# Optimization experiments

Hardware: AMD Instinct MI355X
Metric: run time of the kernel (lower is better)

The kernel has to match this reference:

```python
import jax, jax.numpy as jnp
import numpy as np

IN_DIM = 18 * 2 * 1 * 536  # 19296
H = 512
OUT = 11
STEPS = 1024


def setup_inputs() -> dict:
    key = jax.random.key(0)
    ks = jax.random.split(key, 14)
    s = 0.02  # small init scale for stable LSTM dynamics
    f32 = jnp.float32
    return {
        "inputs": jax.random.normal(ks[0], (STEPS, IN_DIM), dtype=f32),
        "W_in": jax.random.normal(ks[1], (H, IN_DIM), dtype=f32) * s,
        "b_in": jnp.zeros((H,), dtype=f32),
        "Wih0": jax.random.normal(ks[2], (4 * H, H), dtype=f32) * s,
        "Whh0": jax.random.normal(ks[3], (4 * H, H), dtype=f32) * s,
        "bih0": jnp.zeros((4 * H,), dtype=f32),
        "bhh0": jnp.zeros((4 * H,), dtype=f32),
        "Wih1": jax.random.normal(ks[4], (4 * H, H), dtype=f32) * s,
        "Whh1": jax.random.normal(ks[5], (4 * H, H), dtype=f32) * s,
        "bih1": jnp.zeros((4 * H,), dtype=f32),
        "bhh1": jnp.zeros((4 * H,), dtype=f32),
        "W_out": jax.random.normal(ks[6], (OUT, H), dtype=f32) * s,
        "b_out": jnp.zeros((OUT,), dtype=f32),
    }


def _lstm_cell(gates, c):
    # PyTorch gate order: input, forget, cell(g), output
    i, f, g, o = jnp.split(gates, 4, axis=-1)
    c_new = jax.nn.sigmoid(f) * c + jax.nn.sigmoid(i) * jnp.tanh(g)
    h_new = jax.nn.sigmoid(o) * jnp.tanh(c_new)
    return h_new, c_new


def reference(inputs, W_in, b_in, Wih0, Whh0, bih0, bhh0,
              Wih1, Whh1, bih1, bhh1, W_out, b_out):
    # Input projection is time-independent -> batch it across all steps.
    x_proj = inputs @ W_in.T + b_in            # (STEPS, H)
    gx0 = x_proj @ Wih0.T + bih0               # (STEPS, 4H) precomputed layer-0 input gates

    def step(carry, gx0_t):
        h0, c0, h1, c1 = carry
        h0, c0 = _lstm_cell(gx0_t + h0 @ Whh0.T + bhh0, c0)
        h1, c1 = _lstm_cell(h0 @ Wih1.T + bih1 + h1 @ Whh1.T + bhh1, c1)
        return (h0, c0, h1, c1), h1

    z = jnp.zeros((H,), dtype=inputs.dtype)
    (h0, c0, h1, c1), hs = jax.lax.scan(step, (z, z, z, z), gx0)
    outputs = (hs @ W_out.T + b_out)[:, None, :]   # (STEPS, 1, OUT) == torch (steps, batch=1, 11)
    hn = jnp.stack([h0, h1])[:, None, :]           # (num_layers=2, batch=1, H)
    cn = jnp.stack([c0, c1])[:, None, :]
    return outputs, hn, cn
```

## Files before the change

kernel.cpp:

```cpp
#include <hip/hip_runtime.h>
#include <math.h>

typedef unsigned long long ull;
typedef unsigned int u32;
typedef unsigned short u16;
typedef _Float16 half2v __attribute__((ext_vector_type(2)));
typedef __bf16 bf16x8 __attribute__((ext_vector_type(8)));
typedef float f32x4 __attribute__((ext_vector_type(4)));

#define H 512
#define STEPS 1024
#define OUTN 11

__device__ __forceinline__ float sigm(float x) { return 1.f / (1.f + __expf(-x)); }
__device__ __forceinline__ ull ld_pair(const ull* p) {
  return __hip_atomic_load((ull*)p, __ATOMIC_RELAXED, __HIP_MEMORY_SCOPE_AGENT);
}
__device__ __forceinline__ void st_pair(ull* p, ull v) {
  __hip_atomic_store(p, v, __ATOMIC_RELAXED, __HIP_MEMORY_SCOPE_AGENT);
}
__device__ __forceinline__ float dot2acc(half2v a, half2v b, float c) {
#if __has_builtin(__builtin_amdgcn_fdot2)
  return __builtin_amdgcn_fdot2(a, b, c, false);
#else
  return c + (float)a.x * (float)b.x + (float)a.y * (float)b.y;
#endif
}
__device__ __forceinline__ u16 f16bits(float x) {
  return __builtin_bit_cast(u16, (_Float16)x);
}
__device__ __forceinline__ half2v bch2(u32 u) { return __builtin_bit_cast(half2v, u); }

__device__ __forceinline__ u32 split_bf16(float x) {
  u32 u = __float_as_uint(x);
  u32 rh = (u + 0x7FFFu + ((u >> 16) & 1u)) & 0xFFFF0000u;
  float hf = __uint_as_float(rh);
  float lo = x - hf;
  u32 ul = __float_as_uint(lo);
  u32 rl = (ul + 0x7FFFu + ((ul >> 16) & 1u)) & 0xFFFF0000u;
  return (rh >> 16) | rl;
}

__global__ void cvt_split(float* __restrict__ A, float* __restrict__ B, int nA, int n4) {
  int idx = blockIdx.x * 256 + threadIdx.x;
  if (idx >= n4) return;
  int base = idx * 4;
  float* p = (base < nA) ? (A + base) : (B + (base - nA));
  float4 v = *(float4*)p;
  u32 r0 = split_bf16(v.x), r1 = split_bf16(v.y), r2 = split_bf16(v.z), r3 = split_bf16(v.w);
  uint4 o = make_uint4(r0, r1, r2, r3);
  *(uint4*)p = o;
}

__global__ __launch_bounds__(256, 2)
void gemm_hilo(const u32* __restrict__ A2, const u32* __restrict__ B2,
               float* __restrict__ C, int M, int N, int K)
{
  __shared__ __align__(16) u16 Ah[64 * 32], Al[64 * 32], Bh[64 * 32], Bl[64 * 32];
  const int z = blockIdx.z;
  const int zstart = z * 151;
  const int nsteps = (z < 3) ? 151 : 150;
  const int mt = blockIdx.x * 64, nt = blockIdx.y * 64;
  const int tid = threadIdx.x;
  const int row = tid >> 2, cg = (tid & 3) * 8;
  const int wave = tid >> 6, lane = tid & 63;
  const int wm = (wave & 1) * 32, wn = (wave >> 1) * 32;
  const int quad = lane >> 4, l16 = lane & 15;

  f32x4 acc[2][2];
#pragma unroll
  for (int i = 0; i < 2; ++i)
#pragma unroll
    for (int j = 0; j < 2; ++j) acc[i][j] = (f32x4)0.f;

  for (int s = 0; s < nsteps; ++s) {
    const int kb = (zstart + s) * 32;
    {
      const u32* ap = A2 + (size_t)(mt + row) * K + kb + cg;
      const u32* bp = B2 + (size_t)(nt + row) * K + kb + cg;
      uint4 a0 = *(const uint4*)ap, a1 = *(const uint4*)(ap + 4);
      uint4 b0 = *(const uint4*)bp, b1 = *(const uint4*)(bp + 4);
      uint4 hi, lo;
      hi = make_uint4((a0.x & 0xFFFF) | (a0.y << 16), (a0.z & 0xFFFF) | (a0.w << 16),
                      (a1.x & 0xFFFF) | (a1.y << 16), (a1.z & 0xFFFF) | (a1.w << 16));
      lo = make_uint4((a0.x >> 16) | (a0.y & 0xFFFF0000u), (a0.z >> 16) | (a0.w & 0xFFFF0000u),
                      (a1.x >> 16) | (a1.y & 0xFFFF0000u), (a1.z >> 16) | (a1.w & 0xFFFF0000u));
      *(uint4*)&Ah[row * 32 + cg] = hi;
      *(uint4*)&Al[row * 32 + cg] = lo;
      hi = make_uint4((b0.x & 0xFFFF) | (b0.y << 16), (b0.z & 0xFFFF) | (b0.w << 16),
                      (b1.x & 0xFFFF) | (b1.y << 16), (b1.z & 0xFFFF) | (b1.w << 16));
      lo = make_uint4((b0.x >> 16) | (b0.y & 0xFFFF0000u), (b0.z >> 16) | (b0.w & 0xFFFF0000u),
                      (b1.x >> 16) | (b1.y & 0xFFFF0000u), (b1.z >> 16) | (b1.w & 0xFFFF0000u));
      *(uint4*)&Bh[row * 32 + cg] = hi;
      *(uint4*)&Bl[row * 32 + cg] = lo;
    }
    __syncthreads();
    bf16x8 ah[2], al[2], bh[2], bl[2];
#pragma unroll
    for (int mf = 0; mf < 2; ++mf) {
      int r = (wm + mf * 16 + l16) * 32 + quad * 8;
      ah[mf] = *reinterpret_cast<const bf16x8*>(&Ah[r]);
      al[mf] = *reinterpret_cast<const bf16x8*>(&Al[r]);
    }
#pragma unroll
    for (int nf = 0; nf < 2; ++nf) {
      int r = (wn + nf * 16 + l16) * 32 + quad * 8;
      bh[nf] = *reinterpret_cast<const bf16x8*>(&Bh[r]);
      bl[nf] = *reinterpret_cast<const bf16x8*>(&Bl[r]);
    }
#pragma unroll
    for (int mf = 0; mf < 2; ++mf)
#pragma unroll
      for (int nf = 0; nf < 2; ++nf) {
        acc[mf][nf] = __builtin_amdgcn_mfma_f32_16x16x32_bf16(ah[mf], bh[nf], acc[mf][nf], 0, 0, 0);
        acc[mf][nf] = __builtin_amdgcn_mfma_f32_16x16x32_bf16(ah[mf], bl[nf], acc[mf][nf], 0, 0, 0);
        acc[mf][nf] = __builtin_amdgcn_mfma_f32_16x16x32_bf16(al[mf], bh[nf], acc[mf][nf], 0, 0, 0);
      }
    __syncthreads();
  }

#pragma unroll
  for (int mf = 0; mf < 2; ++mf)
#pragma unroll
    for (int nf = 0; nf < 2; ++nf)
#pragma unroll
      for (int r = 0; r < 4; ++r) {
        int rw = mt + wm + mf * 16 + quad * 4 + r;
        int cl = nt + wn + nf * 16 + l16;
        atomicAdd(&C[(size_t)rw * N + cl], acc[mf][nf][r]);
      }
}

#define GBM 64
#define GBN 64
#define GBK 64
#define GLD 76

__global__ __launch_bounds__(256, 2)
void gemm_nt(const float* __restrict__ A, const float* __restrict__ B,
             float* __restrict__ C, const float* __restrict__ bias,
             int M, int N, int K)
{
  __shared__ float As[GBM][GLD];
  __shared__ float Bs[GBN][GLD];
  const int mt = blockIdx.x, nt = blockIdx.y;
  const int tid = threadIdx.x;
  const int tx = tid & 15, ty = tid >> 4;

  float acc[4][4] = {{0.f}};

  for (int kb = 0; kb < K; kb += GBK) {
#pragma unroll
    for (int i = 0; i < 4; ++i) {
      int r = ty + i * 16;
      int gk = kb + tx * 4;
      *(float4*)&As[r][tx * 4] = *(const float4*)(A + (size_t)(mt * GBM + r) * K + gk);
      *(float4*)&Bs[r][tx * 4] = *(const float4*)(B + (size_t)(nt * GBN + r) * K + gk);
    }
    __syncthreads();
#pragma unroll
    for (int k4 = 0; k4 < GBK; k4 += 4) {
      float4 a[4], b[4];
#pragma unroll
      for (int i = 0; i < 4; ++i) a[i] = *(const float4*)&As[ty * 4 + i][k4];
#pragma unroll
      for (int j = 0; j < 4; ++j) b[j] = *(const float4*)&Bs[tx * 4 + j][k4];
#pragma unroll
      for (int i = 0; i < 4; ++i)
#pragma unroll
        for (int j = 0; j < 4; ++j) {
          acc[i][j] = fmaf(a[i].x, b[j].x, acc[i][j]);
          acc[i][j] = fmaf(a[i].y, b[j].y, acc[i][j]);
          acc[i][j] = fmaf(a[i].z, b[j].z, acc[i][j]);
          acc[i][j] = fmaf(a[i].w, b[j].w, acc[i][j]);
        }
    }
    __syncthreads();
  }

#pragma unroll
  for (int i = 0; i < 4; ++i) {
    int m = mt * GBM + ty * 4 + i;
#pragma unroll
    for (int j = 0; j < 4; ++j) {
      int n = nt * GBN + tx * 4 + j;
      C[(size_t)m * N + n] = acc[i][j] + bias[n];
    }
  }
}

__global__ void init_xproj(float* __restrict__ xp, const float* __restrict__ b_in) {
  int i = blockIdx.x * 256 + threadIdx.x;
  xp[i] = b_in[i & (H - 1)];
}

__global__ void out_proj(const float* __restrict__ hs1, const float* __restrict__ Wout,
                         const float* __restrict__ bout, float* __restrict__ out) {
  int idx = blockIdx.x * 256 + threadIdx.x;
  if (idx >= STEPS * OUTN) return;
  int t = idx / OUTN, o = idx - t * OUTN;
  const float* h = hs1 + t * H;
  const float* wr = Wout + o * H;
  float acc = 0.f;
#pragma unroll 4
  for (int i = 0; i < H; i += 4) {
    float4 hv = *(const float4*)(h + i);
    float4 wv = *(const float4*)(wr + i);
    acc = fmaf(hv.x, wv.x, acc);
    acc = fmaf(hv.y, wv.y, acc);
    acc = fmaf(hv.z, wv.z, acc);
    acc = fmaf(hv.w, wv.w, acc);
  }
  out[idx] = acc + bout[o];
}

__global__ __launch_bounds__(512, 1)
void lstm_chains(const float* __restrict__ gx0,
                 const float* __restrict__ Whh0, const float* __restrict__ bhh0,
                 const float* __restrict__ Wih1, const float* __restrict__ Whh1,
                 const float* __restrict__ bih1, const float* __restrict__ bhh1,
                 float* __restrict__ hs1, float* __restrict__ out,
                 ull* __restrict__ hb0, ull* __restrict__ hb1,
                 int* __restrict__ flags1)
{
  const int wg = blockIdx.x;
  const int tid = threadIdx.x;
  const bool role0 = (wg < 8);

  __shared__ __align__(16) u32 hl_u[512];
  __shared__ __align__(16) float gbuf[256];
  __shared__ __align__(16) float gxb[256];

  half2v wgt[8][16];
  float bias[8];
  int rg, ch;

  if (role0) {
    rg = tid >> 4; ch = tid & 15;
    int g = rg >> 3, lub = (rg & 7) * 8;
    int growb = (g << 9) + (wg << 6) + lub;
    const float* wb = Whh0 + (size_t)growb * H + ch * 32;
#pragma unroll
    for (int r = 0; r < 8; ++r) {
      const float* wr = wb + (size_t)r * H;
#pragma unroll
      for (int j4 = 0; j4 < 8; ++j4) {
        float4 f = *(const float4*)(wr + j4 * 4);
        wgt[r][2 * j4]     = half2v{(_Float16)f.x, (_Float16)f.y};
        wgt[r][2 * j4 + 1] = half2v{(_Float16)f.z, (_Float16)f.w};
      }
      bias[r] = bhh0[growb + r];
    }
  } else {
    rg = tid >> 5; ch = tid & 31;
    int g = rg >> 2, lub = (rg & 3) * 8;
    int growb = (g << 9) + ((wg - 8) << 5) + lub;
    const float* wb = (ch < 16) ? (Whh1 + (size_t)growb * H + ch * 32)
                                : (Wih1 + (size_t)growb * H + (ch - 16) * 32);
#pragma unroll
    for (int r = 0; r < 8; ++r) {
      const float* wr = wb + (size_t)r * H;
#pragma unroll
      for (int j4 = 0; j4 < 8; ++j4) {
        float4 f = *(const float4*)(wr + j4 * 4);
        wgt[r][2 * j4]     = half2v{(_Float16)f.x, (_Float16)f.y};
        wgt[r][2 * j4 + 1] = half2v{(_Float16)f.z, (_Float16)f.w};
      }
      bias[r] = bih1[growb + r] + bhh1[growb + r];
    }
  }

  float c_state = 0.f, h_last = 0.f;

  if (role0) {
    const int w = wg;
    for (int t = 0; t < STEPS; ++t) {
      if (tid >= 256) {
        int j = tid - 256;
        gxb[j] = gx0[t * 2048 + ((j >> 6) << 9) + (w << 6) + (j & 63)];
      } else {
        const ull* src = hb0 + (((unsigned)(t + 3) & 3u) << 8) + tid;
        ull p;
        do { p = ld_pair(src); } while ((unsigned)(p >> 32) != (unsigned)t);
        hl_u[tid] = (u32)p;
      }
      __syncthreads();

      float accv[8];
#pragma unroll
      for (int r = 0; r < 8; ++r) accv[r] = 0.f;
      {
        const u32* hp = hl_u + (ch << 4);
        uint4 q0 = *(const uint4*)hp;
        uint4 q1 = *(const uint4*)(hp + 4);
        uint4 q2 = *(const uint4*)(hp + 8);
        uint4 q3 = *(const uint4*)(hp + 12);
        half2v h2[16] = {bch2(q0.x), bch2(q0.y), bch2(q0.z), bch2(q0.w),
                         bch2(q1.x), bch2(q1.y), bch2(q1.z), bch2(q1.w),
                         bch2(q2.x), bch2(q2.y), bch2(q2.z), bch2(q2.w),
                         bch2(q3.x), bch2(q3.y), bch2(q3.z), bch2(q3.w)};
#pragma unroll
        for (int j = 0; j < 16; ++j)
#pragma unroll
          for (int r = 0; r < 8; ++r)
            accv[r] = dot2acc(wgt[r][j], h2[j], accv[r]);
      }
#pragma unroll
      for (int o = 1; o < 16; o <<= 1)
#pragma unroll
        for (int r = 0; r < 8; ++r)
          accv[r] += __shfl_xor(accv[r], o);
      if (ch == 0) {
        float4 ga = *(const float4*)&gxb[rg * 8];
        float4 gb = *(const float4*)&gxb[rg * 8 + 4];
        float4 o0 = make_float4(accv[0] + bias[0] + ga.x, accv[1] + bias[1] + ga.y,
                                accv[2] + bias[2] + ga.z, accv[3] + bias[3] + ga.w);
        float4 o1 = make_float4(accv[4] + bias[4] + gb.x, accv[5] + bias[5] + gb.y,
                                accv[6] + bias[6] + gb.z, accv[7] + bias[7] + gb.w);
        *(float4*)&gbuf[rg * 8] = o0;
        *(float4*)&gbuf[rg * 8 + 4] = o1;
      }
      __syncthreads();

      if (tid < 64) {
        float gi = gbuf[tid], gf = gbuf[64 + tid], gg = gbuf[128 + tid], go = gbuf[192 + tid];
        c_state = sigm(gf) * c_state + sigm(gi) * tanhf(gg);
        float hv = sigm(go) * tanhf(c_state);
        h_last = hv;
        int need = t - 3;
        if (need > 0) {
          int f;
          do {
            f = (tid < 16) ? __hip_atomic_load(&flags1[tid], __ATOMIC_RELAXED,
                                               __HIP_MEMORY_SCOPE_AGENT)
                           : 0x7fffffff;
          } while (!__all(f >= need));
        }
        float hnb = __shfl_down(hv, 1);
        if ((tid & 1) == 0) {
          u32 pay = (u32)f16bits(hv) | ((u32)f16bits(hnb) << 16);
          st_pair(hb0 + (((unsigned)t & 3u) << 8) + (w << 5) + (tid >> 1),
                  ((ull)(unsigned)(t + 1) << 32) | (ull)pay);
        }
      }
    }
  } else {
    const int w1 = wg - 8;
    for (int tau = 1; tau <= STEPS; ++tau) {
      const int t = tau - 1;
      if (tid < 256) {
        const ull* q1 = hb1 + (((unsigned)(t + 3) & 3u) << 8) + tid;
        ull p;
        do { p = ld_pair(q1); } while ((unsigned)(p >> 32) != (unsigned)t);
        hl_u[tid] = (u32)p;
      } else {
        const ull* q0 = hb0 + (((unsigned)t & 3u) << 8) + (tid - 256);
        ull p;
        do { p = ld_pair(q0); } while ((unsigned)(p >> 32) != (unsigned)(t + 1));
        hl_u[tid] = (u32)p;
      }
      __syncthreads();

      float accv[8];
#pragma unroll
      for (int r = 0; r < 8; ++r) accv[r] = 0.f;
      {
        const u32* hp = hl_u + (ch << 4);
        uint4 q0 = *(const uint4*)hp;
        uint4 q1 = *(const uint4*)(hp + 4);
        uint4 q2 = *(const uint4*)(hp + 8);
        uint4 q3 = *(const uint4*)(hp + 12);
        half2v h2[16] = {bch2(q0.x), bch2(q0.y), bch2(q0.z), bch2(q0.w),
                         bch2(q1.x), bch2(q1.y), bch2(q1.z), bch2(q1.w),
                         bch2(q2.x), bch2(q2.y), bch2(q2.z), bch2(q2.w),
                         bch2(q3.x), bch2(q3.y), bch2(q3.z), bch2(q3.w)};
#pragma unroll
        for (int j = 0; j < 16; ++j)
#pragma unroll
          for (int r = 0; r < 8; ++r)
            accv[r] = dot2acc(wgt[r][j], h2[j], accv[r]);
      }
#pragma unroll
      for (int o = 1; o < 32; o <<= 1)
#pragma unroll
        for (int r = 0; r < 8; ++r)
          accv[r] += __shfl_xor(accv[r], o);
      if (ch == 0) {
        float4 o0 = make_float4(accv[0] + bias[0], accv[1] + bias[1],
                                accv[2] + bias[2], accv[3] + bias[3]);
        float4 o1 = make_float4(accv[4] + bias[4], accv[5] + bias[5],
                                accv[6] + bias[6], accv[7] + bias[7]);
        *(float4*)&gbuf[rg * 8] = o0;
        *(float4*)&gbuf[rg * 8 + 4] = o1;
      }
      __syncthreads();

      if (tid < 32) {
        int u = (w1 << 5) + tid;
        float gi = gbuf[tid], gf = gbuf[32 + tid], gg = gbuf[64 + tid], go = gbuf[96 + tid];
        c_state = sigm(gf) * c_state + sigm(gi) * tanhf(gg);
        float hv = sigm(go) * tanhf(c_state);
        h_last = hv;
        hs1[t * H + u] = hv;
        float hnb = __shfl_down(hv, 1);
        if ((tid & 1) == 0) {
          u32 pay = (u32)f16bits(hv) | ((u32)f16bits(hnb) << 16);
          st_pair(hb1 + (((unsigned)t & 3u) << 8) + (w1 << 4) + (tid >> 1),
                  ((ull)(unsigned)(t + 1) << 32) | (ull)pay);
        }
      }
      if (tid == 0)
        __hip_atomic_store(&flags1[w1], tau, __ATOMIC_RELAXED, __HIP_MEMORY_SCOPE_AGENT);
    }
  }

  if (role0) {
    if (tid < 64) {
      int u = (wg << 6) + tid;
      out[STEPS * OUTN + u] = h_last;
      out[STEPS * OUTN + 2 * H + u] = c_state;
    }
  } else {
    if (tid < 32) {
      int u = ((wg - 8) << 5) + tid;
      out[STEPS * OUTN + H + u] = h_last;
      out[STEPS * OUTN + 3 * H + u] = c_state;
    }
  }
}

extern "C" void kernel_launch(void* const* d_in, const int* in_sizes, int n_in,
                              void* d_out, int out_size, void* d_ws, size_t ws_size,
                              hipStream_t stream)
{
  (void)in_sizes; (void)n_in; (void)out_size; (void)ws_size;
  float* inputs = (float*)d_in[0];
  float* W_in   = (float*)d_in[1];
  const float* b_in   = (const float*)d_in[2];
  const float* Wih0   = (const float*)d_in[3];
  const float* Whh0   = (const float*)d_in[4];
  const float* bih0   = (const float*)d_in[5];
  const float* bhh0   = (const float*)d_in[6];
  const float* Wih1   = (const float*)d_in[7];
  const float* Whh1   = (const float*)d_in[8];
  const float* bih1   = (const float*)d_in[9];
  const float* bhh1   = (const float*)d_in[10];
  const float* W_out  = (const float*)d_in[11];
  const float* b_out  = (const float*)d_in[12];
  float* out = (float*)d_out;
  float* ws = (float*)d_ws;

  float* xp  = ws;
  float* gx0 = ws + 524288;
  float* hs1 = ws + 524288 + 2097152;
  char* syncb = (char*)(ws + 3145728);
  ull* hb0 = (ull*)syncb;
  ull* hb1 = (ull*)(syncb + 8192);
  int* flags1 = (int*)(syncb + 16384);

  hipMemsetAsync(syncb, 0, 16448, stream);

  {
    const int nA = STEPS * 19296;
    const int n4 = (nA + H * 19296) / 4;
    cvt_split<<<n4 / 256, 256, 0, stream>>>(inputs, W_in, nA, n4);
  }
  init_xproj<<<2048, 256, 0, stream>>>(xp, b_in);
  {
    dim3 g(16, 8, 4);
    gemm_hilo<<<g, 256, 0, stream>>>((const u32*)inputs, (const u32*)W_in, xp,
                                     1024, 512, 19296);
  }
  {
    dim3 g(16, 32, 1);
    gemm_nt<<<g, 256, 0, stream>>>(xp, Wih0, gx0, bih0, 1024, 2048, 512);
  }
  lstm_chains<<<24, 512, 0, stream>>>(gx0, Whh0, bhh0, Wih1, Whh1, bih1, bhh1,
                                      hs1, out, hb0, hb1, flags1);
  out_proj<<<44, 256, 0, stream>>>(hs1, W_out, b_out, out);
}
```

Before: 3.582 ms.

## Replicate hidden-state mailboxes per consumer and deepen ring to eight slots

```diff
diff --git a/kernel.cpp b/kernel.cpp
--- a/kernel.cpp
+++ b/kernel.cpp
@@ -214,13 +214,17 @@
   out[idx] = acc + bout[o];
 }
 
+#define NC0 24
+#define NC1 16
+#define RD 8
+
 __global__ __launch_bounds__(512, 1)
 void lstm_chains(const float* __restrict__ gx0,
                  const float* __restrict__ Whh0, const float* __restrict__ bhh0,
                  const float* __restrict__ Wih1, const float* __restrict__ Whh1,
                  const float* __restrict__ bih1, const float* __restrict__ bhh1,
                  float* __restrict__ hs1, float* __restrict__ out,
-                 ull* __restrict__ hb0, ull* __restrict__ hb1,
+                 ull* __restrict__ mb0, ull* __restrict__ mb1,
                  int* __restrict__ flags1)
 {
   const int wg = blockIdx.x;
@@ -278,8 +282,14 @@
       if (tid >= 256) {
         int j = tid - 256;
         gxb[j] = gx0[t * 2048 + ((j >> 6) << 9) + (w << 6) + (j & 63)];
+        if (j < 16 && (t & 3) == 0 && t > 0) {
+          int need = t - 4, f;
+          do {
+            f = __hip_atomic_load(&flags1[j], __ATOMIC_RELAXED, __HIP_MEMORY_SCOPE_AGENT);
+          } while (f < need);
+        }
       } else {
-        const ull* src = hb0 + (((unsigned)(t + 3) & 3u) << 8) + tid;
+        const ull* src = mb0 + ((((w << 3) | ((t + RD - 1) & (RD - 1)))) << 8) + tid;
         ull p;
         do { p = ld_pair(src); } while ((unsigned)(p >> 32) != (unsigned)t);
         hl_u[tid] = (u32)p;
@@ -326,35 +336,30 @@
         float gi = gbuf[tid], gf = gbuf[64 + tid], gg = gbuf[128 + tid], go = gbuf[192 + tid];
         c_state = sigm(gf) * c_state + sigm(gi) * tanhf(gg);
         float hv = sigm(go) * tanhf(c_state);
-        h_last = hv;
-        int need = t - 3;
-        if (need > 0) {
-          int f;
-          do {
-            f = (tid < 16) ? __hip_atomic_load(&flags1[tid], __ATOMIC_RELAXED,
-                                               __HIP_MEMORY_SCOPE_AGENT)
-                           : 0x7fffffff;
-          } while (!__all(f >= need));
-        }
         float hnb = __shfl_down(hv, 1);
         if ((tid & 1) == 0) {
-          u32 pay = (u32)f16bits(hv) | ((u32)f16bits(hnb) << 16);
-          st_pair(hb0 + (((unsigned)t & 3u) << 8) + (w << 5) + (tid >> 1),
-                  ((ull)(unsigned)(t + 1) << 32) | (ull)pay);
+          u32 payl = (u32)f16bits(hv) | ((u32)f16bits(hnb) << 16);
+          ull pay = ((ull)(unsigned)(t + 1) << 32) | (ull)payl;
+          const int slot = t & (RD - 1);
+          const int pidx = (w << 5) + (tid >> 1);
+#pragma unroll
+          for (int c = 0; c < NC0; ++c)
+            st_pair(mb0 + (((c << 3) | slot) << 8) + pidx, pay);
         }
+        h_last = hv;
       }
     }
   } else {
-    const int w1 = wg - 8;
+    const int v = wg - 8;
     for (int tau = 1; tau <= STEPS; ++tau) {
       const int t = tau - 1;
       if (tid < 256) {
-        const ull* q1 = hb1 + (((unsigned)(t + 3) & 3u) << 8) + tid;
+        const ull* q1 = mb1 + ((((v << 3) | ((t + RD - 1) & (RD - 1)))) << 8) + tid;
         ull p;
         do { p = ld_pair(q1); } while ((unsigned)(p >> 32) != (unsigned)t);
         hl_u[tid] = (u32)p;
       } else {
-        const ull* q0 = hb0 + (((unsigned)t & 3u) << 8) + (tid - 256);
+        const ull* q0 = mb0 + (((((8 + v) << 3) | (t & (RD - 1)))) << 8) + (tid - 256);
         ull p;
         do { p = ld_pair(q0); } while ((unsigned)(p >> 32) != (unsigned)(t + 1));
         hl_u[tid] = (u32)p;
@@ -396,21 +401,25 @@
       __syncthreads();
 
       if (tid < 32) {
-        int u = (w1 << 5) + tid;
+        int u = (v << 5) + tid;
         float gi = gbuf[tid], gf = gbuf[32 + tid], gg = gbuf[64 + tid], go = gbuf[96 + tid];
         c_state = sigm(gf) * c_state + sigm(gi) * tanhf(gg);
         float hv = sigm(go) * tanhf(c_state);
+        float hnb = __shfl_down(hv, 1);
+        if ((tid & 1) == 0) {
+          u32 payl = (u32)f16bits(hv) | ((u32)f16bits(hnb) << 16);
+          ull pay = ((ull)(unsigned)(t + 1) << 32) | (ull)payl;
+          const int slot = t & (RD - 1);
+          const int pidx = (v << 4) + (tid >> 1);
+#pragma unroll
+          for (int c = 0; c < NC1; ++c)
+            st_pair(mb1 + (((c << 3) | slot) << 8) + pidx, pay);
+        }
         h_last = hv;
         hs1[t * H + u] = hv;
-        float hnb = __shfl_down(hv, 1);
-        if ((tid & 1) == 0) {
-          u32 pay = (u32)f16bits(hv) | ((u32)f16bits(hnb) << 16);
-          st_pair(hb1 + (((unsigned)t & 3u) << 8) + (w1 << 4) + (tid >> 1),
-                  ((ull)(unsigned)(t + 1) << 32) | (ull)pay);
-        }
       }
       if (tid == 0)
-        __hip_atomic_store(&flags1[w1], tau, __ATOMIC_RELAXED, __HIP_MEMORY_SCOPE_AGENT);
+        __hip_atomic_store(&flags1[v], tau, __ATOMIC_RELAXED, __HIP_MEMORY_SCOPE_AGENT);
     }
   }
 
@@ -454,11 +463,11 @@
   float* gx0 = ws + 524288;
   float* hs1 = ws + 524288 + 2097152;
   char* syncb = (char*)(ws + 3145728);
-  ull* hb0 = (ull*)syncb;
-  ull* hb1 = (ull*)(syncb + 8192);
-  int* flags1 = (int*)(syncb + 16384);
-
-  hipMemsetAsync(syncb, 0, 16448, stream);
+  ull* mb0 = (ull*)syncb;
+  ull* mb1 = (ull*)(syncb + 24 * 8 * 256 * 8);
+  int* flags1 = (int*)(syncb + (24 + 16) * 8 * 256 * 8);
+
+  hipMemsetAsync(syncb, 0, (24 + 16) * 8 * 256 * 8 + 64, stream);
 
   {
     const int nA = STEPS * 19296;
@@ -476,6 +485,6 @@
     gemm_nt<<<g, 256, 0, stream>>>(xp, Wih0, gx0, bih0, 1024, 2048, 512);
   }
   lstm_chains<<<24, 512, 0, stream>>>(gx0, Whh0, bhh0, Wih1, Whh1, bih1, bhh1,
-                                      hs1, out, hb0, hb1, flags1);
+                                      hs1, out, mb0, mb1, flags1);
   out_proj<<<44, 256, 0, stream>>>(hs1, W_out, b_out, out);
 }
```

Result: faster. 3.257 ms (-9.1%).
